# Kernel tuning notes

Measured on AMD Instinct MI355X. Metric: run time of the kernel, lower is better.

## Reference

```python
import jax, jax.numpy as jnp
import numpy as np

B, T, IN, H = 1024, 256, 2, 128
H1, H2, H3 = H // 2, H, 2 * H


def _param(key, shape, fan):
    bound = 1.0 / np.sqrt(fan)
    return jax.random.uniform(key, shape, jnp.float32, -bound, bound)


def setup_inputs() -> dict:
    key = jax.random.key(0)
    ks = jax.random.split(key, 16)
    inp = {
        "input": jax.random.normal(ks[0], (B, T, IN), jnp.float32),
        "future": 16,
        # LSTMCell 1: in=IN, hid=H1 (torch gate order i,f,g,o)
        "W_ih1": _param(ks[1], (4 * H1, IN), H1),
        "W_hh1": _param(ks[2], (4 * H1, H1), H1),
        "b_ih1": _param(ks[3], (4 * H1,), H1),
        "b_hh1": _param(ks[4], (4 * H1,), H1),
        # LSTMCell 2: in=H1, hid=H2
        "W_ih2": _param(ks[5], (4 * H2, H1), H2),
        "W_hh2": _param(ks[6], (4 * H2, H2), H2),
        "b_ih2": _param(ks[7], (4 * H2,), H2),
        "b_hh2": _param(ks[8], (4 * H2,), H2),
        # LSTMCell 3: in=H2, hid=H3
        "W_ih3": _param(ks[9], (4 * H3, H2), H3),
        "W_hh3": _param(ks[10], (4 * H3, H3), H3),
        "b_ih3": _param(ks[11], (4 * H3,), H3),
        "b_hh3": _param(ks[12], (4 * H3,), H3),
        # Linear: (H1+H2+H3) -> IN
        "W_lin": _param(ks[13], (IN, H1 + H2 + H3), H1 + H2 + H3),
        "b_lin": _param(ks[14], (IN,), H1 + H2 + H3),
    }
    return inp


def _lstm_cell(x, h, c, Wih, Whh, bih, bhh):
    g = x @ Wih.T + h @ Whh.T + (bih + bhh)
    i, f, gg, o = jnp.split(g, 4, axis=-1)
    c_new = jax.nn.sigmoid(f) * c + jax.nn.sigmoid(i) * jnp.tanh(gg)
    h_new = jax.nn.sigmoid(o) * jnp.tanh(c_new)
    return h_new, c_new


def reference(input, future, W_ih1, W_hh1, b_ih1, b_hh1,
              W_ih2, W_hh2, b_ih2, b_hh2,
              W_ih3, W_hh3, b_ih3, b_hh3, W_lin, b_lin):
    b = input.shape[0]

    def step(state, x):
        h1, c1, h2, c2, h3, c3 = state
        h1, c1 = _lstm_cell(x, h1, c1, W_ih1, W_hh1, b_ih1, b_hh1)
        h2, c2 = _lstm_cell(h1, h2, c2, W_ih2, W_hh2, b_ih2, b_hh2)
        h3, c3 = _lstm_cell(h2, h3, c3, W_ih3, W_hh3, b_ih3, b_hh3)
        out = jnp.concatenate([h1, h2, h3], axis=-1) @ W_lin.T + b_lin
        return (h1, c1, h2, c2, h3, c3), out

    z = lambda d: jnp.zeros((b, d), input.dtype)
    state0 = (z(H1), z(H1), z(H2), z(H2), z(H3), z(H3))

    # consume the input sequence; only the last output is kept (as in torch code)
    def scan_step(state, x):
        state, out = step(state, x)
        return state, out

    state, outs = jax.lax.scan(scan_step, state0, input.transpose(1, 0, 2))
    out = outs[-1]  # [B, IN]

    def fstep(carry, _):
        state, out = carry
        state, out2 = step(state, out)
        return (state, out2), out2

    (_, _), fouts = jax.lax.scan(fstep, (state, out), None, length=future - 1)
    # stack: first kept output + generated ones -> [B, future, IN]
    return jnp.concatenate([out[:, None, :], fouts.transpose(1, 0, 2)], axis=1)
```

## Files before the change

kernel.cpp:

```cpp
#include <hip/hip_runtime.h>


#define T_SEQ 256
#define NREP 32
#define DEPTH 8
#define DMASK 7

#define NJT1 4
#define NJT2 8
#define NJT3 16
#define NKB1 3
#define NKB2 6
#define NKB3 12

#define WSZ1 (NJT1*4*NKB1*512)
#define WSZ2 (NJT2*8*NKB2*256)
#undef WSZ2
#define WSZ2 (NJT2*4*NKB2*512)
#define WSZ3 (NJT3*4*NKB3*512)
#define WTOT (WSZ1+WSZ2+WSZ3)

#define H2_G    (16*128)
#define H2_SLOT (2*H2_G)
#define H2_REP  (DEPTH*H2_SLOT)
#define H3_G    (16*256)
#define H3_SLOT (2*H3_G)
#define H3_REP  (DEPTH*H3_SLOT)

typedef _Float16 half8 __attribute__((ext_vector_type(8)));
typedef _Float16 half4 __attribute__((ext_vector_type(4)));
typedef float f32x4 __attribute__((ext_vector_type(4)));

union H4u { unsigned long long u; half4 h; };
union H8u { unsigned long long u[2]; half8 h; };

__device__ __forceinline__ float sigm(float x) {
  return __fdividef(1.f, 1.f + __expf(-x));
}
__device__ __forceinline__ float tanh_fast(float x) {
  float t = __expf(-2.f * fabsf(x));
  float r = __fdividef(1.f - t, 1.f + t);
  return copysignf(r, x);
}

__device__ __forceinline__ unsigned long long ld64(const _Float16* p) {
  return __hip_atomic_load((const unsigned long long*)p, __ATOMIC_RELAXED,
                           __HIP_MEMORY_SCOPE_SYSTEM);
}
__device__ __forceinline__ half8 ldh8(const _Float16* p) {
  H8u r; r.u[0] = ld64(p); r.u[1] = ld64(p + 4);
  return r.h;
}
__device__ __forceinline__ void st64(_Float16* p, half4 v) {
  H4u r; r.h = v;
  __hip_atomic_store((unsigned long long*)p, r.u, __ATOMIC_RELAXED,
                     __HIP_MEMORY_SCOPE_SYSTEM);
}
__device__ __forceinline__ void stflag(int* p, int v) {
  __hip_atomic_store(p, v, __ATOMIC_RELAXED, __HIP_MEMORY_SCOPE_SYSTEM);
}
__device__ __forceinline__ void wait_rep(int* fb, int t3, int tf) {
  const int lane = threadIdx.x & 63;
  const bool act = (lane < 4) || ((lane == 4) && (tf != (int)0x80000000));
  int* p = fb + (lane < 5 ? lane : 0) * 64;
  const int tg = (lane < 4) ? t3 : tf;
  while (true) {
    int v = 0x7fffffff;
    if (act) v = __hip_atomic_load(p, __ATOMIC_RELAXED, __HIP_MEMORY_SCOPE_SYSTEM);
    if (__all(v >= tg)) break;
    __builtin_amdgcn_s_sleep(1);
  }
  asm volatile("" ::: "memory");
}

__global__ void prep_weights(const float* __restrict__ Wih1, const float* __restrict__ Whh1,
                             const float* __restrict__ Wih2, const float* __restrict__ Whh2,
                             const float* __restrict__ Wih3, const float* __restrict__ Whh3,
                             _Float16* __restrict__ WT) {
  int idx = blockIdx.x * blockDim.x + threadIdx.x;
  if (idx >= WTOT) return;
  float v = 0.f;
  if (idx < WSZ1) {
    const int e = idx, blk = e >> 9, wb = e & 511;
    const int lane = wb >> 3, j = wb & 7;
    const int tl = blk / NKB1, kk = blk % NKB1;
    const int q = tl / NJT1, jt = tl % NJT1;
    const int r = q * 64 + jt * 16 + (lane & 15);
    const int k = kk * 32 + ((lane >> 4) << 3) + j;
    if (k < 64)       v = Whh1[r * 64 + k];
    else if (k < 66)  v = Wih1[r * 2 + (k - 64)];
  } else if (idx < WSZ1 + WSZ2) {
    const int e = idx - WSZ1, blk = e >> 9, wb = e & 511;
    const int lane = wb >> 3, j = wb & 7;
    const int tl = blk / NKB2, kk = blk % NKB2;
    const int q = tl / NJT2, jt = tl % NJT2;
    const int r = q * 128 + jt * 16 + (lane & 15);
    const int k = kk * 32 + ((lane >> 4) << 3) + j;
    if (k < 64)       v = Wih2[r * 64 + k];
    else              v = Whh2[r * 128 + (k - 64)];
  } else {
    const int e = idx - WSZ1 - WSZ2, blk = e >> 9, wb = e & 511;
    const int lane = wb >> 3, j = wb & 7;
    const int tl = blk / NKB3, kk = blk % NKB3;
    const int q = tl / NJT3, jt = tl % NJT3;
    const int r = q * 256 + jt * 16 + (lane & 15);
    const int k = kk * 32 + ((lane >> 4) << 3) + j;
    if (k < 128)      v = Wih3[r * 128 + k];
    else              v = Whh3[r * 256 + (k - 128)];
  }
  WT[idx] = (_Float16)v;
}

__global__ __launch_bounds__(256, 1) void pipe_main(
    const float* __restrict__ input, const int* __restrict__ future_p,
    const float* __restrict__ bih1, const float* __restrict__ bhh1,
    const float* __restrict__ bih2, const float* __restrict__ bhh2,
    const float* __restrict__ bih3, const float* __restrict__ bhh3,
    const float* __restrict__ Wlin, const float* __restrict__ blin,
    const _Float16* __restrict__ WT,
    _Float16* __restrict__ h2r, _Float16* __restrict__ h3r,
    int* __restrict__ flags,
    float* __restrict__ out) {
  __shared__ __align__(16) _Float16 xh1[2][16][96];
  __shared__ __align__(16) _Float16 xh2[2][16][192];
  __shared__ float wlin[2][448];

  const int fut = *future_p;
  const int nsteps = T_SEQ - 1 + fut;

  const int rep = blockIdx.x % NREP;
  const int role = blockIdx.x / NREP;

  int* fb = flags + rep * 512;
  const int NEG = (int)0x80000000;

  const int tid = threadIdx.x;
  const int w = tid >> 6, lane = tid & 63;
  const int n = lane & 15, l4 = lane >> 4;

  _Float16* h2b = h2r + (size_t)rep * H2_REP;
  _Float16* h3b = h3r + (size_t)rep * H3_REP;

  if (role == 0) {
    for (int i = tid; i < 2*16*96;  i += 256) (&xh1[0][0][0])[i] = (_Float16)0.f;
    for (int i = tid; i < 2*16*192; i += 256) (&xh2[0][0][0])[i] = (_Float16)0.f;
    for (int i = tid; i < 896; i += 256) (&wlin[0][0])[i] = Wlin[i];

    half8 a1[4][3];
#pragma unroll
    for (int q = 0; q < 4; ++q)
#pragma unroll
      for (int kk = 0; kk < 3; ++kk)
        a1[q][kk] = *(const half8*)(WT + ((q*NJT1 + w)*NKB1 + kk)*512 + lane*8);
    half8 a2[2][4][6];
#pragma unroll
    for (int u = 0; u < 2; ++u)
#pragma unroll
      for (int q = 0; q < 4; ++q)
#pragma unroll
        for (int kk = 0; kk < 6; ++kk)
          a2[u][q][kk] = *(const half8*)(WT + WSZ1 + ((q*NJT2 + (u*4+w))*NKB2 + kk)*512 + lane*8);
    float b1[4][4], b2[2][4][4];
#pragma unroll
    for (int q = 0; q < 4; ++q)
#pragma unroll
      for (int e = 0; e < 4; ++e) {
        const int r1 = q*64 + w*16 + l4*4 + e;
        b1[q][e] = bih1[r1] + bhh1[r1];
#pragma unroll
        for (int u = 0; u < 2; ++u) {
          const int r2 = q*128 + (u*4+w)*16 + l4*4 + e;
          b2[u][q][e] = bih2[r2] + bhh2[r2];
        }
      }
    float c1[2][4] = {}, c2[2][2][4] = {};
    __syncthreads();

    for (int it = 0; it <= nsteps; ++it) {
      const int tp = it - 1;
      const int tg3 = (it >= T_SEQ) ? it : it - 6;
      wait_rep(fb, tg3, NEG);

      if (tp >= T_SEQ - 1 && tid < 128) {
        const int kq = tid & 1, ch = (tid >> 1) & 1, nn = (tid >> 2) & 15, gl = (tid >> 6) & 1;
        const _Float16* h3p = h3b + (size_t)(tp & DMASK)*H3_SLOT + gl*H3_G + nn*256;
        float acc = 0.f;
        for (int k = kq*224; k < kq*224 + 224; k += 4) {
          half4 xv;
          if (k < 192) xv = *(const half4*)(&xh2[gl][nn][k]);
          else         { H4u u; u.u = ld64(h3p + (k - 192)); xv = u.h; }
          const float* wl = &wlin[ch][k];
          acc = fmaf(wl[0], (float)xv[0], acc);
          acc = fmaf(wl[1], (float)xv[1], acc);
          acc = fmaf(wl[2], (float)xv[2], acc);
          acc = fmaf(wl[3], (float)xv[3], acc);
        }
        acc += __shfl_xor(acc, 1, 64);
        if (kq == 0) {
          const float o = acc + blin[ch];
          out[((size_t)(rep*32 + gl*16 + nn)*fut + (tp - (T_SEQ - 1)))*2 + ch] = o;
          xh1[gl][nn][64 + ch] = (_Float16)o;
        }
      }
      if (it < T_SEQ && tid < 64) {
        const int gl = tid >> 5, nn = (tid >> 1) & 15, ch = tid & 1;
        xh1[gl][nn][64 + ch] =
            (_Float16)input[((size_t)(rep*32 + gl*16 + nn)*T_SEQ + it)*2 + ch];
      }
      __syncthreads();
      if (it == nsteps) break;

      half8 bf1[2][3];
#pragma unroll
      for (int g = 0; g < 2; ++g)
#pragma unroll
        for (int kk = 0; kk < 3; ++kk)
          bf1[g][kk] = *(const half8*)(&xh1[g][n][kk*32 + l4*8]);
      __syncthreads();
#pragma unroll
      for (int g = 0; g < 2; ++g) {
        f32x4 acc[4];
#pragma unroll
        for (int q = 0; q < 4; ++q)
#pragma unroll
          for (int e = 0; e < 4; ++e) acc[q][e] = b1[q][e];
#pragma unroll
        for (int q = 0; q < 4; ++q)
#pragma unroll
          for (int kk = 0; kk < 3; ++kk)
            acc[q] = __builtin_amdgcn_mfma_f32_16x16x32_f16(a1[q][kk], bf1[g][kk], acc[q], 0, 0, 0);
        half4 hv;
#pragma unroll
        for (int e = 0; e < 4; ++e) {
          const float cn = sigm(acc[1][e]) * c1[g][e] + sigm(acc[0][e]) * tanh_fast(acc[2][e]);
          const float h = sigm(acc[3][e]) * tanh_fast(cn);
          c1[g][e] = cn;
          hv[e] = (_Float16)h;
        }
        *(half4*)(&xh1[g][n][w*16 + l4*4]) = hv;
        *(half4*)(&xh2[g][n][w*16 + l4*4]) = hv;
      }
      __syncthreads();

      half8 bf2[2][6];
#pragma unroll
      for (int g = 0; g < 2; ++g)
#pragma unroll
        for (int kk = 0; kk < 6; ++kk)
          bf2[g][kk] = *(const half8*)(&xh2[g][n][kk*32 + l4*8]);
      __syncthreads();
      const int slot = it & DMASK;
#pragma unroll
      for (int u = 0; u < 2; ++u)
#pragma unroll
        for (int g = 0; g < 2; ++g) {
          f32x4 acc[4];
#pragma unroll
          for (int q = 0; q < 4; ++q)
#pragma unroll
            for (int e = 0; e < 4; ++e) acc[q][e] = b2[u][q][e];
#pragma unroll
          for (int q = 0; q < 4; ++q)
#pragma unroll
            for (int kk = 0; kk < 6; ++kk)
              acc[q] = __builtin_amdgcn_mfma_f32_16x16x32_f16(a2[u][q][kk], bf2[g][kk], acc[q], 0, 0, 0);
          half4 hv;
#pragma unroll
          for (int e = 0; e < 4; ++e) {
            const float cn = sigm(acc[1][e]) * c2[u][g][e] + sigm(acc[0][e]) * tanh_fast(acc[2][e]);
            const float h = sigm(acc[3][e]) * tanh_fast(cn);
            c2[u][g][e] = cn;
            hv[e] = (_Float16)h;
          }
          const int row = (u*4 + w)*16 + l4*4;
          *(half4*)(&xh2[g][n][64 + row]) = hv;
          st64(h2b + (size_t)slot*H2_SLOT + g*H2_G + n*128 + row, hv);
        }
      asm volatile("s_waitcnt vmcnt(0)" ::: "memory");
      __syncthreads();
      if (tid == 0) stflag(fb + 4*64, it + 1);
    }
  } else {
    const int slice = role - 1;
    const int tl = slice*4 + w;
    half8 a3[4][12];
#pragma unroll
    for (int q = 0; q < 4; ++q)
#pragma unroll
      for (int kk = 0; kk < 12; ++kk)
        a3[q][kk] = *(const half8*)(WT + WSZ1 + WSZ2 + ((q*NJT3 + tl)*NKB3 + kk)*512 + lane*8);
    float b3[4][4];
#pragma unroll
    for (int q = 0; q < 4; ++q)
#pragma unroll
      for (int e = 0; e < 4; ++e) {
        const int r = q*256 + tl*16 + l4*4 + e;
        b3[q][e] = bih3[r] + bhh3[r];
      }
    float c3[2][4] = {};

    for (int t = 0; t < nsteps; ++t) {
      wait_rep(fb, t, t + 1);
      const int slot = t & DMASK, slot1 = (t - 1) & DMASK;
      half8 bf[2][12];
#pragma unroll
      for (int g = 0; g < 2; ++g) {
        const _Float16* h2p = h2b + (size_t)slot*H2_SLOT + g*H2_G + n*128;
#pragma unroll
        for (int kk = 0; kk < 4; ++kk) bf[g][kk] = ldh8(h2p + kk*32 + l4*8);
        if (t > 0) {
          const _Float16* h3p = h3b + (size_t)slot1*H3_SLOT + g*H3_G + n*256;
#pragma unroll
          for (int kk = 4; kk < 12; ++kk) bf[g][kk] = ldh8(h3p + (kk-4)*32 + l4*8);
        } else {
#pragma unroll
          for (int kk = 4; kk < 12; ++kk) bf[g][kk] = half8{};
        }
      }
#pragma unroll
      for (int g = 0; g < 2; ++g) {
        f32x4 acc[4];
#pragma unroll
        for (int q = 0; q < 4; ++q)
#pragma unroll
          for (int e = 0; e < 4; ++e) acc[q][e] = b3[q][e];
#pragma unroll
        for (int q = 0; q < 4; ++q)
#pragma unroll
          for (int kk = 0; kk < 12; ++kk)
            acc[q] = __builtin_amdgcn_mfma_f32_16x16x32_f16(a3[q][kk], bf[g][kk], acc[q], 0, 0, 0);
        half4 hv;
#pragma unroll
        for (int e = 0; e < 4; ++e) {
          const float cn = sigm(acc[1][e]) * c3[g][e] + sigm(acc[0][e]) * tanh_fast(acc[2][e]);
          const float h = sigm(acc[3][e]) * tanh_fast(cn);
          c3[g][e] = cn;
          hv[e] = (_Float16)h;
        }
        st64(h3b + (size_t)slot*H3_SLOT + g*H3_G + n*256 + tl*16 + l4*4, hv);
      }
      asm volatile("s_waitcnt vmcnt(0)" ::: "memory");
      __syncthreads();
      if (tid == 0) stflag(fb + slice*64, t + 1);
    }
  }
}

extern "C" void kernel_launch(void* const* d_in, const int* in_sizes, int n_in,
                              void* d_out, int out_size, void* d_ws, size_t ws_size,
                              hipStream_t stream) {
  const float* input = (const float*)d_in[0];
  const int*   fut   = (const int*)d_in[1];
  const float* Wih1  = (const float*)d_in[2];
  const float* Whh1  = (const float*)d_in[3];
  const float* bih1  = (const float*)d_in[4];
  const float* bhh1  = (const float*)d_in[5];
  const float* Wih2  = (const float*)d_in[6];
  const float* Whh2  = (const float*)d_in[7];
  const float* bih2  = (const float*)d_in[8];
  const float* bhh2  = (const float*)d_in[9];
  const float* Wih3  = (const float*)d_in[10];
  const float* Whh3  = (const float*)d_in[11];
  const float* bih3  = (const float*)d_in[12];
  const float* bhh3  = (const float*)d_in[13];
  const float* Wlin  = (const float*)d_in[14];
  const float* blin  = (const float*)d_in[15];
  float* out = (float*)d_out;

  _Float16* WT  = (_Float16*)d_ws;
  _Float16* h2r = WT + WTOT;
  _Float16* h3r = h2r + (size_t)NREP * H2_REP;
  int* flags    = (int*)(h3r + (size_t)NREP * H3_REP);
  const size_t flag_bytes = (size_t)NREP * 512 * sizeof(int);

  prep_weights<<<(WTOT + 255) / 256, 256, 0, stream>>>(Wih1, Whh1, Wih2, Whh2, Wih3, Whh3, WT);
  hipMemsetAsync(flags, 0, flag_bytes, stream);
  pipe_main<<<5 * NREP, 256, 0, stream>>>(input, fut,
                                          bih1, bhh1, bih2, bhh2, bih3, bhh3,
                                          Wlin, blin, WT, h2r, h3r, flags, out);
}
```

Before: 2.267 ms.

## Split layer-3 across two sibling blocks per team with LDS staging and partial linear

Reorganizes the pipelined LSTM from five blocks per replica (one layer-1/2 block plus four layer-3 slices) to three blocks per team, where two blocks each own half of layer 3 with doubled MFMA tiles per wave. The h3 state each block produced is kept in LDS, and the sibling half is staged through shared memory. Each layer-3 block computes its part of the output linear and publishes it for the layer-1/2 block to combine. Flag waits for layer 1/2 are batched every 4 steps, and a spin cap with a dead flag is added. This lowers inter-block flag traffic and the number of global h3 loads, at the cost of heavier per-block work and extra __syncthreads.

```diff
diff --git a/kernel.cpp b/kernel.cpp
--- a/kernel.cpp
+++ b/kernel.cpp
@@ -2,9 +2,8 @@
 
 
 #define T_SEQ 256
-#define NREP 32
-#define DEPTH 8
-#define DMASK 7
+#define NTEAM 32
+#define G2 2
 
 #define NJT1 4
 #define NJT2 8
@@ -14,25 +13,22 @@
 #define NKB3 12
 
 #define WSZ1 (NJT1*4*NKB1*512)
-#define WSZ2 (NJT2*8*NKB2*256)
-#undef WSZ2
 #define WSZ2 (NJT2*4*NKB2*512)
 #define WSZ3 (NJT3*4*NKB3*512)
 #define WTOT (WSZ1+WSZ2+WSZ3)
 
-#define H2_G    (16*128)
-#define H2_SLOT (2*H2_G)
-#define H2_REP  (DEPTH*H2_SLOT)
-#define H3_G    (16*256)
-#define H3_SLOT (2*H3_G)
-#define H3_REP  (DEPTH*H3_SLOT)
+#define H2SLOT 4096
+#define H2TEAM (8*H2SLOT)
+#define H3SLOT 8192
+#define H3TEAM (4*H3SLOT)
+#define PRTEAM 512
+#define CAP_WAIT (1<<22)
 
 typedef _Float16 half8 __attribute__((ext_vector_type(8)));
 typedef _Float16 half4 __attribute__((ext_vector_type(4)));
 typedef float f32x4 __attribute__((ext_vector_type(4)));
 
 union H4u { unsigned long long u; half4 h; };
-union H8u { unsigned long long u[2]; half8 h; };
 
 __device__ __forceinline__ float sigm(float x) {
   return __fdividef(1.f, 1.f + __expf(-x));
@@ -43,34 +39,43 @@
   return copysignf(r, x);
 }
 
-__device__ __forceinline__ unsigned long long ld64(const _Float16* p) {
+__device__ __forceinline__ unsigned long long ld64p(const _Float16* p) {
   return __hip_atomic_load((const unsigned long long*)p, __ATOMIC_RELAXED,
                            __HIP_MEMORY_SCOPE_SYSTEM);
 }
-__device__ __forceinline__ half8 ldh8(const _Float16* p) {
-  H8u r; r.u[0] = ld64(p); r.u[1] = ld64(p + 4);
-  return r.h;
-}
-__device__ __forceinline__ void st64(_Float16* p, half4 v) {
+__device__ __forceinline__ void st64p(_Float16* p, half4 v) {
   H4u r; r.h = v;
   __hip_atomic_store((unsigned long long*)p, r.u, __ATOMIC_RELAXED,
                      __HIP_MEMORY_SCOPE_SYSTEM);
 }
+__device__ __forceinline__ float ldfp(const float* p) {
+  return __hip_atomic_load(p, __ATOMIC_RELAXED, __HIP_MEMORY_SCOPE_SYSTEM);
+}
+__device__ __forceinline__ void stfp(float* p, float v) {
+  __hip_atomic_store(p, v, __ATOMIC_RELAXED, __HIP_MEMORY_SCOPE_SYSTEM);
+}
 __device__ __forceinline__ void stflag(int* p, int v) {
-  __hip_atomic_store(p, v, __ATOMIC_RELAXED, __HIP_MEMORY_SCOPE_SYSTEM);
-}
-__device__ __forceinline__ void wait_rep(int* fb, int t3, int tf) {
+  __hip_atomic_store(p, v, __ATOMIC_RELEASE, __HIP_MEMORY_SCOPE_SYSTEM);
+}
+__device__ __forceinline__ void wait2(const int* pA, int tA, const int* pB, int tB,
+                                      volatile int* dead) {
+  if (*dead) return;
   const int lane = threadIdx.x & 63;
-  const bool act = (lane < 4) || ((lane == 4) && (tf != (int)0x80000000));
-  int* p = fb + (lane < 5 ? lane : 0) * 64;
-  const int tg = (lane < 4) ? t3 : tf;
+  const int* p = (lane == 1) ? pB : pA;
+  const int tg = (lane == 0) ? tA : (lane == 1 ? tB : (int)0x80000000);
+  int iter = 0;
   while (true) {
-    int v = 0x7fffffff;
-    if (act) v = __hip_atomic_load(p, __ATOMIC_RELAXED, __HIP_MEMORY_SCOPE_SYSTEM);
+    const int v = (lane < 2)
+        ? __hip_atomic_load(p, __ATOMIC_RELAXED, __HIP_MEMORY_SCOPE_SYSTEM)
+        : 0x7fffffff;
     if (__all(v >= tg)) break;
+    if (++iter > CAP_WAIT) { if (lane == 0) *dead = 1; break; }
     __builtin_amdgcn_s_sleep(1);
   }
   asm volatile("" ::: "memory");
+}
+__device__ __forceinline__ void vm0() {
+  asm volatile("s_waitcnt vmcnt(0)" ::: "memory");
 }
 
 __global__ void prep_weights(const float* __restrict__ Wih1, const float* __restrict__ Whh1,
@@ -119,32 +124,42 @@
     const float* __restrict__ Wlin, const float* __restrict__ blin,
     const _Float16* __restrict__ WT,
     _Float16* __restrict__ h2r, _Float16* __restrict__ h3r,
-    int* __restrict__ flags,
+    float* __restrict__ pr, int* __restrict__ flags,
     float* __restrict__ out) {
-  __shared__ __align__(16) _Float16 xh1[2][16][96];
-  __shared__ __align__(16) _Float16 xh2[2][16][192];
-  __shared__ float wlin[2][448];
-
-  const int fut = *future_p;
-  const int nsteps = T_SEQ - 1 + fut;
-
-  const int rep = blockIdx.x % NREP;
-  const int role = blockIdx.x / NREP;
-
-  int* fb = flags + rep * 512;
-  const int NEG = (int)0x80000000;
-
   const int tid = threadIdx.x;
   const int w = tid >> 6, lane = tid & 63;
   const int n = lane & 15, l4 = lane >> 4;
 
-  _Float16* h2b = h2r + (size_t)rep * H2_REP;
-  _Float16* h3b = h3r + (size_t)rep * H3_REP;
+  const int team = blockIdx.x & 31;
+  const int role = blockIdx.x >> 5;
+  const int b0 = team * 32;
+
+  const int fut = *future_p;
+  const int nsteps = T_SEQ - 1 + fut;
+
+  int* fbase = flags + team * 192;
+  int* fA = fbase;
+  int* fB = fbase + 64;
+  int* fF = fbase + 128;
+  _Float16* h2b = h2r + (size_t)team * H2TEAM;
+  _Float16* h3b = h3r + (size_t)team * H3TEAM;
+  float* prb = pr + (size_t)team * PRTEAM;
+
+  __shared__ volatile int sh_dead;
+  if (tid == 0) sh_dead = 0;
 
   if (role == 0) {
-    for (int i = tid; i < 2*16*96;  i += 256) (&xh1[0][0][0])[i] = (_Float16)0.f;
-    for (int i = tid; i < 2*16*192; i += 256) (&xh2[0][0][0])[i] = (_Float16)0.f;
-    for (int i = tid; i < 896; i += 256) (&wlin[0][0])[i] = Wlin[i];
+    __shared__ __align__(16) _Float16 xh1s[G2][16][104];
+    __shared__ __align__(16) _Float16 xh2s[G2][16][200];
+    __shared__ float bs1[256], bs2[512], wlinF[2][192], blin_s[2];
+
+    for (int i = tid; i < G2*16*104; i += 256) (&xh1s[0][0][0])[i] = (_Float16)0.f;
+    for (int i = tid; i < G2*16*200; i += 256) (&xh2s[0][0][0])[i] = (_Float16)0.f;
+    if (tid < 256) bs1[tid] = bih1[tid] + bhh1[tid];
+    bs2[tid] = bih2[tid] + bhh2[tid];
+    bs2[tid + 256] = bih2[tid + 256] + bhh2[tid + 256];
+    if (tid < 192) { wlinF[0][tid] = Wlin[tid]; wlinF[1][tid] = Wlin[448 + tid]; }
+    if (tid < 2) blin_s[tid] = blin[tid];
 
     half8 a1[4][3];
 #pragma unroll
@@ -160,70 +175,57 @@
 #pragma unroll
         for (int kk = 0; kk < 6; ++kk)
           a2[u][q][kk] = *(const half8*)(WT + WSZ1 + ((q*NJT2 + (u*4+w))*NKB2 + kk)*512 + lane*8);
-    float b1[4][4], b2[2][4][4];
-#pragma unroll
-    for (int q = 0; q < 4; ++q)
-#pragma unroll
-      for (int e = 0; e < 4; ++e) {
-        const int r1 = q*64 + w*16 + l4*4 + e;
-        b1[q][e] = bih1[r1] + bhh1[r1];
-#pragma unroll
-        for (int u = 0; u < 2; ++u) {
-          const int r2 = q*128 + (u*4+w)*16 + l4*4 + e;
-          b2[u][q][e] = bih2[r2] + bhh2[r2];
-        }
-      }
-    float c1[2][4] = {}, c2[2][2][4] = {};
+    float c1[G2][4] = {}, c2[2][G2][4] = {};
     __syncthreads();
 
     for (int it = 0; it <= nsteps; ++it) {
       const int tp = it - 1;
-      const int tg3 = (it >= T_SEQ) ? it : it - 6;
-      wait_rep(fb, tg3, NEG);
-
-      if (tp >= T_SEQ - 1 && tid < 128) {
-        const int kq = tid & 1, ch = (tid >> 1) & 1, nn = (tid >> 2) & 15, gl = (tid >> 6) & 1;
-        const _Float16* h3p = h3b + (size_t)(tp & DMASK)*H3_SLOT + gl*H3_G + nn*256;
+      if (it >= T_SEQ)        wait2(fA, it, fB, it, &sh_dead);
+      else if ((it & 3) == 0) wait2(fA, it - 4, fB, it - 4, &sh_dead);
+
+      if (tp >= T_SEQ - 1) {
+        const int g = w >> 1, ch = w & 1;
+        const int kq = l4;
         float acc = 0.f;
-        for (int k = kq*224; k < kq*224 + 224; k += 4) {
-          half4 xv;
-          if (k < 192) xv = *(const half4*)(&xh2[gl][nn][k]);
-          else         { H4u u; u.u = ld64(h3p + (k - 192)); xv = u.h; }
-          const float* wl = &wlin[ch][k];
+#pragma unroll
+        for (int i = 0; i < 12; ++i) {
+          const int k = kq*48 + i*4;
+          const half4 xv = *(const half4*)(&xh2s[g][n][k]);
+          const float* wl = &wlinF[ch][k];
           acc = fmaf(wl[0], (float)xv[0], acc);
           acc = fmaf(wl[1], (float)xv[1], acc);
           acc = fmaf(wl[2], (float)xv[2], acc);
           acc = fmaf(wl[3], (float)xv[3], acc);
         }
-        acc += __shfl_xor(acc, 1, 64);
-        if (kq == 0) {
-          const float o = acc + blin[ch];
-          out[((size_t)(rep*32 + gl*16 + nn)*fut + (tp - (T_SEQ - 1)))*2 + ch] = o;
-          xh1[gl][nn][64 + ch] = (_Float16)o;
+        acc += __shfl_xor(acc, 16, 64);
+        acc += __shfl_xor(acc, 32, 64);
+        if (l4 == 0) {
+          const float* pp = prb + (tp & 3)*128 + g*32 + n*2 + ch;
+          const float o = acc + blin_s[ch] + ldfp(pp) + ldfp(pp + 64);
+          out[((size_t)(b0 + g*16 + n)*fut + (tp - (T_SEQ - 1)))*2 + ch] = o;
+          xh1s[g][n][64 + ch] = (_Float16)o;
         }
       }
       if (it < T_SEQ && tid < 64) {
-        const int gl = tid >> 5, nn = (tid >> 1) & 15, ch = tid & 1;
-        xh1[gl][nn][64 + ch] =
-            (_Float16)input[((size_t)(rep*32 + gl*16 + nn)*T_SEQ + it)*2 + ch];
+        const int g = tid >> 5, nn = (tid >> 1) & 15, ch = tid & 1;
+        xh1s[g][nn][64 + ch] =
+            (_Float16)input[((size_t)(b0 + g*16 + nn)*T_SEQ + it)*2 + ch];
       }
       __syncthreads();
       if (it == nsteps) break;
 
-      half8 bf1[2][3];
-#pragma unroll
-      for (int g = 0; g < 2; ++g)
+      half8 bf1[G2][3];
+#pragma unroll
+      for (int g = 0; g < G2; ++g)
 #pragma unroll
         for (int kk = 0; kk < 3; ++kk)
-          bf1[g][kk] = *(const half8*)(&xh1[g][n][kk*32 + l4*8]);
-      __syncthreads();
-#pragma unroll
-      for (int g = 0; g < 2; ++g) {
+          bf1[g][kk] = *(const half8*)(&xh1s[g][n][kk*32 + l4*8]);
+      __syncthreads();
+#pragma unroll
+      for (int g = 0; g < G2; ++g) {
         f32x4 acc[4];
 #pragma unroll
-        for (int q = 0; q < 4; ++q)
-#pragma unroll
-          for (int e = 0; e < 4; ++e) acc[q][e] = b1[q][e];
+        for (int q = 0; q < 4; ++q) acc[q] = *(const f32x4*)(&bs1[q*64 + w*16 + l4*4]);
 #pragma unroll
         for (int q = 0; q < 4; ++q)
 #pragma unroll
@@ -237,28 +239,27 @@
           c1[g][e] = cn;
           hv[e] = (_Float16)h;
         }
-        *(half4*)(&xh1[g][n][w*16 + l4*4]) = hv;
-        *(half4*)(&xh2[g][n][w*16 + l4*4]) = hv;
-      }
-      __syncthreads();
-
-      half8 bf2[2][6];
-#pragma unroll
-      for (int g = 0; g < 2; ++g)
+        *(half4*)(&xh1s[g][n][w*16 + l4*4]) = hv;
+        *(half4*)(&xh2s[g][n][w*16 + l4*4]) = hv;
+      }
+      __syncthreads();
+
+      half8 bf2[G2][6];
+#pragma unroll
+      for (int g = 0; g < G2; ++g)
 #pragma unroll
         for (int kk = 0; kk < 6; ++kk)
-          bf2[g][kk] = *(const half8*)(&xh2[g][n][kk*32 + l4*8]);
-      __syncthreads();
-      const int slot = it & DMASK;
+          bf2[g][kk] = *(const half8*)(&xh2s[g][n][kk*32 + l4*8]);
+      __syncthreads();
+      const int slot = it & 7;
 #pragma unroll
       for (int u = 0; u < 2; ++u)
 #pragma unroll
-        for (int g = 0; g < 2; ++g) {
+        for (int g = 0; g < G2; ++g) {
           f32x4 acc[4];
 #pragma unroll
           for (int q = 0; q < 4; ++q)
-#pragma unroll
-            for (int e = 0; e < 4; ++e) acc[q][e] = b2[u][q][e];
+            acc[q] = *(const f32x4*)(&bs2[q*128 + (u*4+w)*16 + l4*4]);
 #pragma unroll
           for (int q = 0; q < 4; ++q)
 #pragma unroll
@@ -273,75 +274,134 @@
             hv[e] = (_Float16)h;
           }
           const int row = (u*4 + w)*16 + l4*4;
-          *(half4*)(&xh2[g][n][64 + row]) = hv;
-          st64(h2b + (size_t)slot*H2_SLOT + g*H2_G + n*128 + row, hv);
-        }
-      asm volatile("s_waitcnt vmcnt(0)" ::: "memory");
-      __syncthreads();
-      if (tid == 0) stflag(fb + 4*64, it + 1);
+          *(half4*)(&xh2s[g][n][64 + row]) = hv;
+          st64p(h2b + (size_t)slot*H2SLOT + g*2048 + n*128 + row, hv);
+        }
+      vm0();
+      __syncthreads();
+      if (tid == 0) stflag(fF, it + 1);
     }
   } else {
-    const int slice = role - 1;
-    const int tl = slice*4 + w;
-    half8 a3[4][12];
-#pragma unroll
-    for (int q = 0; q < 4; ++q)
-#pragma unroll
-      for (int kk = 0; kk < 12; ++kk)
-        a3[q][kk] = *(const half8*)(WT + WSZ1 + WSZ2 + ((q*NJT3 + tl)*NKB3 + kk)*512 + lane*8);
-    float b3[4][4];
-#pragma unroll
-    for (int q = 0; q < 4; ++q)
-#pragma unroll
-      for (int e = 0; e < 4; ++e) {
-        const int r = q*256 + tl*16 + l4*4 + e;
-        b3[q][e] = bih3[r] + bhh3[r];
-      }
-    float c3[2][4] = {};
+    const int h = role - 1, hs = 1 - h;
+    __shared__ __align__(16) _Float16 stage[G2][16][264];
+    __shared__ __align__(16) _Float16 xh3own[G2][16][132];
+    __shared__ float bs3s[4][2][4][16];
+    __shared__ float wlp[2][128];
+
+    for (int i = tid; i < G2*16*264; i += 256) (&stage[0][0][0])[i] = (_Float16)0.f;
+    for (int i = tid; i < G2*16*132; i += 256) (&xh3own[0][0][0])[i] = (_Float16)0.f;
+    {
+      int i = tid;
+#pragma unroll
+      for (int rnd = 0; rnd < 2; ++rnd, i += 256) {
+        const int w2 = i >> 7, u = (i >> 6) & 1, q = (i >> 4) & 3, col = i & 15;
+        const int r = q*256 + (h*8 + w2*2 + u)*16 + col;
+        bs3s[w2][u][q][col] = bih3[r] + bhh3[r];
+      }
+    }
+    if (tid < 256) {
+      const int ch = tid >> 7, k = tid & 127;
+      wlp[ch][k] = Wlin[ch*448 + 192 + h*128 + k];
+    }
+    half8 a3[2][4][12];
+#pragma unroll
+    for (int u = 0; u < 2; ++u)
+#pragma unroll
+      for (int q = 0; q < 4; ++q)
+#pragma unroll
+        for (int kk = 0; kk < 12; ++kk)
+          a3[u][q][kk] = *(const half8*)(WT + WSZ1 + WSZ2 +
+              ((q*NJT3 + (h*8 + w*2 + u))*NKB3 + kk)*512 + lane*8);
+    float c3[G2][2][4] = {};
+    int* fme  = h ? fB : fA;
+    int* fsib = h ? fA : fB;
+    __syncthreads();
 
     for (int t = 0; t < nsteps; ++t) {
-      wait_rep(fb, t, t + 1);
-      const int slot = t & DMASK, slot1 = (t - 1) & DMASK;
-      half8 bf[2][12];
-#pragma unroll
-      for (int g = 0; g < 2; ++g) {
-        const _Float16* h2p = h2b + (size_t)slot*H2_SLOT + g*H2_G + n*128;
-#pragma unroll
-        for (int kk = 0; kk < 4; ++kk) bf[g][kk] = ldh8(h2p + kk*32 + l4*8);
-        if (t > 0) {
-          const _Float16* h3p = h3b + (size_t)slot1*H3_SLOT + g*H3_G + n*256;
-#pragma unroll
-          for (int kk = 4; kk < 12; ++kk) bf[g][kk] = ldh8(h3p + (kk-4)*32 + l4*8);
-        } else {
-#pragma unroll
-          for (int kk = 4; kk < 12; ++kk) bf[g][kk] = half8{};
-        }
-      }
-#pragma unroll
-      for (int g = 0; g < 2; ++g) {
-        f32x4 acc[4];
-#pragma unroll
-        for (int q = 0; q < 4; ++q)
-#pragma unroll
-          for (int e = 0; e < 4; ++e) acc[q][e] = b3[q][e];
-#pragma unroll
-        for (int q = 0; q < 4; ++q)
-#pragma unroll
-          for (int kk = 0; kk < 12; ++kk)
-            acc[q] = __builtin_amdgcn_mfma_f32_16x16x32_f16(a3[q][kk], bf[g][kk], acc[q], 0, 0, 0);
-        half4 hv;
-#pragma unroll
-        for (int e = 0; e < 4; ++e) {
-          const float cn = sigm(acc[1][e]) * c3[g][e] + sigm(acc[0][e]) * tanh_fast(acc[2][e]);
-          const float h = sigm(acc[3][e]) * tanh_fast(cn);
-          c3[g][e] = cn;
-          hv[e] = (_Float16)h;
-        }
-        st64(h3b + (size_t)slot*H3_SLOT + g*H3_G + n*256 + tl*16 + l4*4, hv);
-      }
-      asm volatile("s_waitcnt vmcnt(0)" ::: "memory");
-      __syncthreads();
-      if (tid == 0) stflag(fb + slice*64, t + 1);
+      wait2(fsib, t, fF, t + 1, &sh_dead);
+      const int s2 = t & 7, s3 = (t - 1) & 3;
+#pragma unroll
+      for (int g = 0; g < G2; ++g) {
+        half8 bfo[4];
+#pragma unroll
+        for (int s = 0; s < 4; ++s)
+          bfo[s] = *(const half8*)(&xh3own[g][n][s*32 + l4*8]);
+#pragma unroll
+        for (int j = 0; j < 2; ++j) {
+          const int kst = 2*w + j;
+          H4u v0, v1;
+          if (kst < 4) {
+            const _Float16* p = h2b + (size_t)s2*H2SLOT + g*2048 + n*128 + kst*32 + l4*8;
+            v0.u = ld64p(p); v1.u = ld64p(p + 4);
+          } else if (t > 0) {
+            const _Float16* p = h3b + (size_t)s3*H3SLOT + hs*4096 + g*2048 + n*128
+                              + (kst - 4)*32 + l4*8;
+            v0.u = ld64p(p); v1.u = ld64p(p + 4);
+          } else { v0.u = 0; v1.u = 0; }
+          *(half4*)(&stage[g][n][kst*32 + l4*8]) = v0.h;
+          *(half4*)(&stage[g][n][kst*32 + l4*8 + 4]) = v1.h;
+        }
+        __syncthreads();
+        half8 bf[12];
+#pragma unroll
+        for (int s = 0; s < 4; ++s) {
+          bf[s] = *(const half8*)(&stage[g][n][s*32 + l4*8]);
+          bf[4 + 4*h + s] = bfo[s];
+          bf[4 + 4*hs + s] = *(const half8*)(&stage[g][n][128 + s*32 + l4*8]);
+        }
+        f32x4 acc[2][4];
+#pragma unroll
+        for (int u = 0; u < 2; ++u)
+#pragma unroll
+          for (int q = 0; q < 4; ++q)
+            acc[u][q] = *(const f32x4*)(&bs3s[w][u][q][l4*4]);
+#pragma unroll
+        for (int u = 0; u < 2; ++u)
+#pragma unroll
+          for (int q = 0; q < 4; ++q)
+#pragma unroll
+            for (int kk = 0; kk < 12; ++kk)
+              acc[u][q] = __builtin_amdgcn_mfma_f32_16x16x32_f16(a3[u][q][kk], bf[kk], acc[u][q], 0, 0, 0);
+#pragma unroll
+        for (int u = 0; u < 2; ++u) {
+          half4 hv;
+#pragma unroll
+          for (int e = 0; e < 4; ++e) {
+            const float cn = sigm(acc[u][1][e]) * c3[g][u][e]
+                           + sigm(acc[u][0][e]) * tanh_fast(acc[u][2][e]);
+            const float hh = sigm(acc[u][3][e]) * tanh_fast(cn);
+            c3[g][u][e] = cn;
+            hv[e] = (_Float16)hh;
+          }
+          const int c = (w*2 + u)*16 + l4*4;
+          *(half4*)(&xh3own[g][n][c]) = hv;
+          st64p(h3b + (size_t)(t & 3)*H3SLOT + h*4096 + g*2048 + n*128 + c, hv);
+        }
+        __syncthreads();
+      }
+      vm0();
+      __syncthreads();
+      if (t >= T_SEQ - 1) {
+        const int g = w >> 1, ch = w & 1;
+        float pa = 0.f;
+#pragma unroll
+        for (int i = 0; i < 8; ++i) {
+          const int k = l4*32 + i*4;
+          const half4 xv = *(const half4*)(&xh3own[g][n][k]);
+          const float* wl = &wlp[ch][k];
+          pa = fmaf(wl[0], (float)xv[0], pa);
+          pa = fmaf(wl[1], (float)xv[1], pa);
+          pa = fmaf(wl[2], (float)xv[2], pa);
+          pa = fmaf(wl[3], (float)xv[3], pa);
+        }
+        pa += __shfl_xor(pa, 16, 64);
+        pa += __shfl_xor(pa, 32, 64);
+        if (l4 == 0)
+          stfp(prb + (t & 3)*128 + h*64 + g*32 + n*2 + ch, pa);
+        vm0();
+        __syncthreads();
+      }
+      if (tid == 0) stflag(fme, t + 1);
     }
   }
 }
@@ -369,13 +429,14 @@
 
   _Float16* WT  = (_Float16*)d_ws;
   _Float16* h2r = WT + WTOT;
-  _Float16* h3r = h2r + (size_t)NREP * H2_REP;
-  int* flags    = (int*)(h3r + (size_t)NREP * H3_REP);
-  const size_t flag_bytes = (size_t)NREP * 512 * sizeof(int);
+  _Float16* h3r = h2r + (size_t)NTEAM * H2TEAM;
+  float*    pr  = (float*)(h3r + (size_t)NTEAM * H3TEAM);
+  int*    flags = (int*)(pr + (size_t)NTEAM * PRTEAM);
+  const size_t flag_bytes = (size_t)NTEAM * 192 * sizeof(int);
 
   prep_weights<<<(WTOT + 255) / 256, 256, 0, stream>>>(Wih1, Whh1, Wih2, Whh2, Wih3, Whh3, WT);
   hipMemsetAsync(flags, 0, flag_bytes, stream);
-  pipe_main<<<5 * NREP, 256, 0, stream>>>(input, fut,
-                                          bih1, bhh1, bih2, bhh2, bih3, bhh3,
-                                          Wlin, blin, WT, h2r, h3r, flags, out);
-}
+  pipe_main<<<96, 256, 0, stream>>>(input, fut,
+                                    bih1, bhh1, bih2, bhh2, bih3, bhh3,
+                                    Wlin, blin, WT, h2r, h3r, pr, flags, out);
+}
```

Result: slower. 3.656 ms (+61.3%).

## Regroup pipeline into 16 teams of 64 rows with per-wave flags and layer-3 partial projections

Applied to the files above, without the earlier changes.

Replaces 32 replicas of 32 batch rows with 16 teams of 64 rows, so each block handles four 16-row groups. The grid shrinks from 160 to 80 blocks and per-team weight-load overhead is amortized over more rows. Layer-3 blocks now double-buffer their global h2/h3 loads across groups and compute the output-projection partials for their own h3 slice. This removes the serial 448-wide dot product from the layer-1/2 block. Synchronization moves to per-wave flags with a bounded wait cap, and the ring depth and lookahead drop from 8/6 to 4/3. The trade-off is more serial work per block on fewer CUs, and a wait cap that can silently give up on a stalled producer.

```diff
diff --git a/kernel.cpp b/kernel.cpp
--- a/kernel.cpp
+++ b/kernel.cpp
@@ -2,9 +2,9 @@
 
 
 #define T_SEQ 256
-#define NREP 32
-#define DEPTH 8
-#define DMASK 7
+#define NTEAM 16
+#define G4 4
+#define DEPTH 4
 
 #define NJT1 4
 #define NJT2 8
@@ -12,20 +12,16 @@
 #define NKB1 3
 #define NKB2 6
 #define NKB3 12
-
 #define WSZ1 (NJT1*4*NKB1*512)
-#define WSZ2 (NJT2*8*NKB2*256)
-#undef WSZ2
 #define WSZ2 (NJT2*4*NKB2*512)
 #define WSZ3 (NJT3*4*NKB3*512)
 #define WTOT (WSZ1+WSZ2+WSZ3)
 
-#define H2_G    (16*128)
-#define H2_SLOT (2*H2_G)
-#define H2_REP  (DEPTH*H2_SLOT)
-#define H3_G    (16*256)
-#define H3_SLOT (2*H3_G)
-#define H3_REP  (DEPTH*H3_SLOT)
+#define H2_TEAM (G4*DEPTH*2048)
+#define H3_TEAM (G4*DEPTH*4096)
+#define PR_TEAM (G4*DEPTH*4*32)
+#define FL_TEAM 1088
+#define CAP_WAIT (1<<22)
 
 typedef _Float16 half8 __attribute__((ext_vector_type(8)));
 typedef _Float16 half4 __attribute__((ext_vector_type(4)));
@@ -43,31 +39,37 @@
   return copysignf(r, x);
 }
 
-__device__ __forceinline__ unsigned long long ld64(const _Float16* p) {
+__device__ __forceinline__ unsigned long long ld64p(const _Float16* p) {
   return __hip_atomic_load((const unsigned long long*)p, __ATOMIC_RELAXED,
                            __HIP_MEMORY_SCOPE_SYSTEM);
 }
-__device__ __forceinline__ half8 ldh8(const _Float16* p) {
-  H8u r; r.u[0] = ld64(p); r.u[1] = ld64(p + 4);
-  return r.h;
-}
-__device__ __forceinline__ void st64(_Float16* p, half4 v) {
+__device__ __forceinline__ void st64p(_Float16* p, half4 v) {
   H4u r; r.h = v;
   __hip_atomic_store((unsigned long long*)p, r.u, __ATOMIC_RELAXED,
                      __HIP_MEMORY_SCOPE_SYSTEM);
 }
+__device__ __forceinline__ float ldfp(const float* p) {
+  return __hip_atomic_load(p, __ATOMIC_RELAXED, __HIP_MEMORY_SCOPE_SYSTEM);
+}
+__device__ __forceinline__ void stfp(float* p, float v) {
+  __hip_atomic_store(p, v, __ATOMIC_RELAXED, __HIP_MEMORY_SCOPE_SYSTEM);
+}
 __device__ __forceinline__ void stflag(int* p, int v) {
   __hip_atomic_store(p, v, __ATOMIC_RELAXED, __HIP_MEMORY_SCOPE_SYSTEM);
 }
-__device__ __forceinline__ void wait_rep(int* fb, int t3, int tf) {
+__device__ __forceinline__ void vm0() {
+  asm volatile("s_waitcnt vmcnt(0)" ::: "memory");
+}
+__device__ __forceinline__ void waitq(const int* ft, int tg3, int tgF, int* dead) {
+  if (*dead) return;
   const int lane = threadIdx.x & 63;
-  const bool act = (lane < 4) || ((lane == 4) && (tf != (int)0x80000000));
-  int* p = fb + (lane < 5 ? lane : 0) * 64;
-  const int tg = (lane < 4) ? t3 : tf;
+  const int* p = ft + ((lane < 17) ? lane : 0) * 64;
+  const int tg = (lane < 16) ? tg3 : (lane == 16 ? tgF : (int)0x80000000);
+  int it = 0;
   while (true) {
-    int v = 0x7fffffff;
-    if (act) v = __hip_atomic_load(p, __ATOMIC_RELAXED, __HIP_MEMORY_SCOPE_SYSTEM);
+    const int v = __hip_atomic_load(p, __ATOMIC_RELAXED, __HIP_MEMORY_SCOPE_SYSTEM);
     if (__all(v >= tg)) break;
+    if (++it > CAP_WAIT) { *dead = 1; break; }
     __builtin_amdgcn_s_sleep(1);
   }
   asm volatile("" ::: "memory");
@@ -111,6 +113,63 @@
   WT[idx] = (_Float16)v;
 }
 
+#define LOADQ(bf, g, t)                                                        \
+  {                                                                            \
+    const _Float16* p2_ = h2b + (((g)*DEPTH + ((t)&3)) << 11) + n*128 + l4*8;  \
+    _Pragma("unroll")                                                          \
+    for (int kk_ = 0; kk_ < 4; ++kk_) {                                        \
+      H8u u_; u_.u[0] = ld64p(p2_ + kk_*32); u_.u[1] = ld64p(p2_ + kk_*32 + 4);\
+      bf[kk_] = u_.h;                                                          \
+    }                                                                          \
+    if ((t) > 0) {                                                             \
+      const _Float16* p3_ = h3b + (((g)*DEPTH + (((t)-1)&3)) << 12)            \
+                          + n*256 + l4*8;                                      \
+      _Pragma("unroll")                                                        \
+      for (int s_ = 0; s_ < 8; ++s_) {                                         \
+        H8u u_; u_.u[0] = ld64p(p3_ + s_*32); u_.u[1] = ld64p(p3_ + s_*32 + 4);\
+        bf[4 + s_] = u_.h;                                                     \
+      }                                                                        \
+    } else {                                                                   \
+      _Pragma("unroll")                                                        \
+      for (int s_ = 0; s_ < 8; ++s_) bf[4 + s_] = half8{};                     \
+    }                                                                          \
+  }
+
+#define COMPUTEQ(bf, g, t, futp)                                               \
+  {                                                                            \
+    f32x4 acc_[4];                                                             \
+    _Pragma("unroll")                                                          \
+    for (int q_ = 0; q_ < 4; ++q_)                                             \
+      _Pragma("unroll")                                                        \
+      for (int e_ = 0; e_ < 4; ++e_) acc_[q_][e_] = b3r[q_][e_];               \
+    _Pragma("unroll")                                                          \
+    for (int q_ = 0; q_ < 4; ++q_)                                             \
+      _Pragma("unroll")                                                        \
+      for (int kk_ = 0; kk_ < 12; ++kk_)                                       \
+        acc_[q_] = __builtin_amdgcn_mfma_f32_16x16x32_f16(a3[q_][kk_], bf[kk_],\
+                                                          acc_[q_], 0, 0, 0); \
+    half4 hv_; float hf_[4];                                                   \
+    _Pragma("unroll")                                                          \
+    for (int e_ = 0; e_ < 4; ++e_) {                                           \
+      const float cn_ = sigm(acc_[1][e_]) * c3[g][e_]                          \
+                      + sigm(acc_[0][e_]) * tanh_fast(acc_[2][e_]);            \
+      hf_[e_] = sigm(acc_[3][e_]) * tanh_fast(cn_);                            \
+      c3[g][e_] = cn_;                                                         \
+      hv_[e_] = (_Float16)hf_[e_];                                             \
+    }                                                                          \
+    st64p(h3b + (((g)*DEPTH + ((t)&3)) << 12) + n*256 + tl*16 + l4*4, hv_);    \
+    if (futp) {                                                                \
+      float p0_ = 0.f, p1_ = 0.f;                                              \
+      _Pragma("unroll")                                                        \
+      for (int e_ = 0; e_ < 4; ++e_) {                                         \
+        p0_ = fmaf(wle[0][e_], hf_[e_], p0_);                                  \
+        p1_ = fmaf(wle[1][e_], hf_[e_], p1_);                                  \
+      }                                                                        \
+      part[g][n][0][(w << 2) | l4] = p0_;                                      \
+      part[g][n][1][(w << 2) | l4] = p1_;                                      \
+    }                                                                          \
+  }
+
 __global__ __launch_bounds__(256, 1) void pipe_main(
     const float* __restrict__ input, const int* __restrict__ future_p,
     const float* __restrict__ bih1, const float* __restrict__ bhh1,
@@ -119,32 +178,34 @@
     const float* __restrict__ Wlin, const float* __restrict__ blin,
     const _Float16* __restrict__ WT,
     _Float16* __restrict__ h2r, _Float16* __restrict__ h3r,
-    int* __restrict__ flags,
+    float* __restrict__ pr, int* __restrict__ flags,
     float* __restrict__ out) {
-  __shared__ __align__(16) _Float16 xh1[2][16][96];
-  __shared__ __align__(16) _Float16 xh2[2][16][192];
-  __shared__ float wlin[2][448];
-
-  const int fut = *future_p;
-  const int nsteps = T_SEQ - 1 + fut;
-
-  const int rep = blockIdx.x % NREP;
-  const int role = blockIdx.x / NREP;
-
-  int* fb = flags + rep * 512;
-  const int NEG = (int)0x80000000;
+  __shared__ __align__(16) _Float16 xh1s[G4][16][104];
+  __shared__ __align__(16) _Float16 xh2s[G4][16][200];
+  __shared__ float wlinF[2][192];
+  __shared__ float part[G4][16][2][16];
 
   const int tid = threadIdx.x;
   const int w = tid >> 6, lane = tid & 63;
   const int n = lane & 15, l4 = lane >> 4;
-
-  _Float16* h2b = h2r + (size_t)rep * H2_REP;
-  _Float16* h3b = h3r + (size_t)rep * H3_REP;
+  const int team = blockIdx.x % NTEAM;
+  const int role = blockIdx.x / NTEAM;
+  const int b0 = team * 64;
+  const int fut = *future_p;
+  const int nsteps = T_SEQ - 1 + fut;
+  int* ft = flags + team * FL_TEAM;
+  int* flf = ft + 16 * 64;
+  _Float16* h2b = h2r + (size_t)team * H2_TEAM;
+  _Float16* h3b = h3r + (size_t)team * H3_TEAM;
+  float* prb = pr + (size_t)team * PR_TEAM;
+  int dead = 0;
+  const int NEG = (int)0x80000000;
 
   if (role == 0) {
-    for (int i = tid; i < 2*16*96;  i += 256) (&xh1[0][0][0])[i] = (_Float16)0.f;
-    for (int i = tid; i < 2*16*192; i += 256) (&xh2[0][0][0])[i] = (_Float16)0.f;
-    for (int i = tid; i < 896; i += 256) (&wlin[0][0])[i] = Wlin[i];
+    for (int i = tid; i < G4*16*104; i += 256) (&xh1s[0][0][0])[i] = (_Float16)0.f;
+    for (int i = tid; i < G4*16*200; i += 256) (&xh2s[0][0][0])[i] = (_Float16)0.f;
+    for (int i = tid; i < 384; i += 256)
+      wlinF[i / 192][i % 192] = Wlin[(i / 192) * 448 + (i % 192)];
 
     half8 a1[4][3];
 #pragma unroll
@@ -160,70 +221,69 @@
 #pragma unroll
         for (int kk = 0; kk < 6; ++kk)
           a2[u][q][kk] = *(const half8*)(WT + WSZ1 + ((q*NJT2 + (u*4+w))*NKB2 + kk)*512 + lane*8);
-    float b1[4][4], b2[2][4][4];
+    float b1r[4][4], b2r[2][4][4];
 #pragma unroll
     for (int q = 0; q < 4; ++q)
 #pragma unroll
       for (int e = 0; e < 4; ++e) {
         const int r1 = q*64 + w*16 + l4*4 + e;
-        b1[q][e] = bih1[r1] + bhh1[r1];
+        b1r[q][e] = bih1[r1] + bhh1[r1];
 #pragma unroll
         for (int u = 0; u < 2; ++u) {
           const int r2 = q*128 + (u*4+w)*16 + l4*4 + e;
-          b2[u][q][e] = bih2[r2] + bhh2[r2];
+          b2r[u][q][e] = bih2[r2] + bhh2[r2];
         }
       }
-    float c1[2][4] = {}, c2[2][2][4] = {};
+    float c1[G4][4] = {}, c2[2][G4][4] = {};
     __syncthreads();
 
     for (int it = 0; it <= nsteps; ++it) {
       const int tp = it - 1;
-      const int tg3 = (it >= T_SEQ) ? it : it - 6;
-      wait_rep(fb, tg3, NEG);
+      waitq(ft, (it >= T_SEQ) ? it : it - 3, NEG, &dead);
 
       if (tp >= T_SEQ - 1 && tid < 128) {
-        const int kq = tid & 1, ch = (tid >> 1) & 1, nn = (tid >> 2) & 15, gl = (tid >> 6) & 1;
-        const _Float16* h3p = h3b + (size_t)(tp & DMASK)*H3_SLOT + gl*H3_G + nn*256;
+        const int g = tid >> 5, nn = (tid >> 1) & 15, ch = tid & 1;
         float acc = 0.f;
-        for (int k = kq*224; k < kq*224 + 224; k += 4) {
-          half4 xv;
-          if (k < 192) xv = *(const half4*)(&xh2[gl][nn][k]);
-          else         { H4u u; u.u = ld64(h3p + (k - 192)); xv = u.h; }
-          const float* wl = &wlin[ch][k];
+#pragma unroll
+        for (int i = 0; i < 48; ++i) {
+          const int k = i * 4;
+          const half4 xv = *(const half4*)(&xh2s[g][nn][k]);
+          const float* wl = &wlinF[ch][k];
           acc = fmaf(wl[0], (float)xv[0], acc);
           acc = fmaf(wl[1], (float)xv[1], acc);
           acc = fmaf(wl[2], (float)xv[2], acc);
           acc = fmaf(wl[3], (float)xv[3], acc);
         }
-        acc += __shfl_xor(acc, 1, 64);
-        if (kq == 0) {
-          const float o = acc + blin[ch];
-          out[((size_t)(rep*32 + gl*16 + nn)*fut + (tp - (T_SEQ - 1)))*2 + ch] = o;
-          xh1[gl][nn][64 + ch] = (_Float16)o;
-        }
-      }
-      if (it < T_SEQ && tid < 64) {
-        const int gl = tid >> 5, nn = (tid >> 1) & 15, ch = tid & 1;
-        xh1[gl][nn][64 + ch] =
-            (_Float16)input[((size_t)(rep*32 + gl*16 + nn)*T_SEQ + it)*2 + ch];
-      }
+        const int sl = tp & 3;
+#pragma unroll
+        for (int q = 0; q < 4; ++q)
+          acc += ldfp(prb + ((g*DEPTH + sl)*4 + q)*32 + nn*2 + ch);
+        const float o = acc + blin[ch];
+        out[((size_t)(b0 + g*16 + nn)*fut + (tp - (T_SEQ - 1)))*2 + ch] = o;
+        xh1s[g][nn][64 + ch] = (_Float16)o;
+      }
+      if (it < T_SEQ && tid < 128) {
+        const int g = tid >> 5, nn = (tid >> 1) & 15, ch = tid & 1;
+        xh1s[g][nn][64 + ch] =
+            (_Float16)input[((size_t)(b0 + g*16 + nn)*T_SEQ + it)*2 + ch];
+      }
+      if (it == nsteps) break;
       __syncthreads();
-      if (it == nsteps) break;
-
-      half8 bf1[2][3];
-#pragma unroll
-      for (int g = 0; g < 2; ++g)
+
+      half8 bf1[G4][3];
+#pragma unroll
+      for (int g = 0; g < G4; ++g)
 #pragma unroll
         for (int kk = 0; kk < 3; ++kk)
-          bf1[g][kk] = *(const half8*)(&xh1[g][n][kk*32 + l4*8]);
+          bf1[g][kk] = *(const half8*)(&xh1s[g][n][kk*32 + l4*8]);
       __syncthreads();
 #pragma unroll
-      for (int g = 0; g < 2; ++g) {
+      for (int g = 0; g < G4; ++g) {
         f32x4 acc[4];
 #pragma unroll
         for (int q = 0; q < 4; ++q)
 #pragma unroll
-          for (int e = 0; e < 4; ++e) acc[q][e] = b1[q][e];
+          for (int e = 0; e < 4; ++e) acc[q][e] = b1r[q][e];
 #pragma unroll
         for (int q = 0; q < 4; ++q)
 #pragma unroll
@@ -237,28 +297,28 @@
           c1[g][e] = cn;
           hv[e] = (_Float16)h;
         }
-        *(half4*)(&xh1[g][n][w*16 + l4*4]) = hv;
-        *(half4*)(&xh2[g][n][w*16 + l4*4]) = hv;
+        *(half4*)(&xh1s[g][n][w*16 + l4*4]) = hv;
+        *(half4*)(&xh2s[g][n][w*16 + l4*4]) = hv;
       }
       __syncthreads();
 
-      half8 bf2[2][6];
-#pragma unroll
-      for (int g = 0; g < 2; ++g)
+      half8 bf2[G4][6];
+#pragma unroll
+      for (int g = 0; g < G4; ++g)
 #pragma unroll
         for (int kk = 0; kk < 6; ++kk)
-          bf2[g][kk] = *(const half8*)(&xh2[g][n][kk*32 + l4*8]);
+          bf2[g][kk] = *(const half8*)(&xh2s[g][n][kk*32 + l4*8]);
       __syncthreads();
-      const int slot = it & DMASK;
+      const int slot = it & 3;
 #pragma unroll
       for (int u = 0; u < 2; ++u)
 #pragma unroll
-        for (int g = 0; g < 2; ++g) {
+        for (int g = 0; g < G4; ++g) {
           f32x4 acc[4];
 #pragma unroll
           for (int q = 0; q < 4; ++q)
 #pragma unroll
-            for (int e = 0; e < 4; ++e) acc[q][e] = b2[u][q][e];
+            for (int e = 0; e < 4; ++e) acc[q][e] = b2r[u][q][e];
 #pragma unroll
           for (int q = 0; q < 4; ++q)
 #pragma unroll
@@ -273,75 +333,66 @@
             hv[e] = (_Float16)h;
           }
           const int row = (u*4 + w)*16 + l4*4;
-          *(half4*)(&xh2[g][n][64 + row]) = hv;
-          st64(h2b + (size_t)slot*H2_SLOT + g*H2_G + n*128 + row, hv);
+          *(half4*)(&xh2s[g][n][64 + row]) = hv;
+          st64p(h2b + ((g*DEPTH + slot) << 11) + n*128 + row, hv);
         }
-      asm volatile("s_waitcnt vmcnt(0)" ::: "memory");
+      vm0();
       __syncthreads();
-      if (tid == 0) stflag(fb + 4*64, it + 1);
+      if (tid == 0) stflag(flf, it + 1);
     }
   } else {
-    const int slice = role - 1;
-    const int tl = slice*4 + w;
+    const int qh = role - 1;
+    const int tl = qh*4 + w;
     half8 a3[4][12];
 #pragma unroll
     for (int q = 0; q < 4; ++q)
 #pragma unroll
       for (int kk = 0; kk < 12; ++kk)
         a3[q][kk] = *(const half8*)(WT + WSZ1 + WSZ2 + ((q*NJT3 + tl)*NKB3 + kk)*512 + lane*8);
-    float b3[4][4];
+    float b3r[4][4], wle[2][4];
 #pragma unroll
     for (int q = 0; q < 4; ++q)
 #pragma unroll
       for (int e = 0; e < 4; ++e) {
         const int r = q*256 + tl*16 + l4*4 + e;
-        b3[q][e] = bih3[r] + bhh3[r];
-      }
-    float c3[2][4] = {};
+        b3r[q][e] = bih3[r] + bhh3[r];
+      }
+#pragma unroll
+    for (int ch = 0; ch < 2; ++ch)
+#pragma unroll
+      for (int e = 0; e < 4; ++e)
+        wle[ch][e] = Wlin[ch*448 + 192 + tl*16 + l4*4 + e];
+    float c3[G4][4] = {};
+    half8 bfA[12], bfB[12];
 
     for (int t = 0; t < nsteps; ++t) {
-      wait_rep(fb, t, t + 1);
-      const int slot = t & DMASK, slot1 = (t - 1) & DMASK;
-      half8 bf[2][12];
-#pragma unroll
-      for (int g = 0; g < 2; ++g) {
-        const _Float16* h2p = h2b + (size_t)slot*H2_SLOT + g*H2_G + n*128;
-#pragma unroll
-        for (int kk = 0; kk < 4; ++kk) bf[g][kk] = ldh8(h2p + kk*32 + l4*8);
-        if (t > 0) {
-          const _Float16* h3p = h3b + (size_t)slot1*H3_SLOT + g*H3_G + n*256;
-#pragma unroll
-          for (int kk = 4; kk < 12; ++kk) bf[g][kk] = ldh8(h3p + (kk-4)*32 + l4*8);
-        } else {
-#pragma unroll
-          for (int kk = 4; kk < 12; ++kk) bf[g][kk] = half8{};
+      waitq(ft, t, t + 1, &dead);
+      const bool futp = (t >= T_SEQ - 1);
+
+      LOADQ(bfA, 0, t);
+      LOADQ(bfB, 1, t);
+      __builtin_amdgcn_sched_barrier(0);
+      COMPUTEQ(bfA, 0, t, futp);
+      LOADQ(bfA, 2, t);
+      __builtin_amdgcn_sched_barrier(0);
+      COMPUTEQ(bfB, 1, t, futp);
+      LOADQ(bfB, 3, t);
+      __builtin_amdgcn_sched_barrier(0);
+      COMPUTEQ(bfA, 2, t, futp);
+      COMPUTEQ(bfB, 3, t, futp);
+
+      if (futp) {
+        __syncthreads();
+        if (tid < 128) {
+          const int g = tid >> 5, nn = (tid >> 1) & 15, ch = tid & 1;
+          float s = 0.f;
+#pragma unroll
+          for (int j = 0; j < 16; ++j) s += part[g][nn][ch][j];
+          stfp(prb + ((g*DEPTH + (t & 3))*4 + qh)*32 + nn*2 + ch, s);
         }
       }
-#pragma unroll
-      for (int g = 0; g < 2; ++g) {
-        f32x4 acc[4];
-#pragma unroll
-        for (int q = 0; q < 4; ++q)
-#pragma unroll
-          for (int e = 0; e < 4; ++e) acc[q][e] = b3[q][e];
-#pragma unroll
-        for (int q = 0; q < 4; ++q)
-#pragma unroll
-          for (int kk = 0; kk < 12; ++kk)
-            acc[q] = __builtin_amdgcn_mfma_f32_16x16x32_f16(a3[q][kk], bf[g][kk], acc[q], 0, 0, 0);
-        half4 hv;
-#pragma unroll
-        for (int e = 0; e < 4; ++e) {
-          const float cn = sigm(acc[1][e]) * c3[g][e] + sigm(acc[0][e]) * tanh_fast(acc[2][e]);
-          const float h = sigm(acc[3][e]) * tanh_fast(cn);
-          c3[g][e] = cn;
-          hv[e] = (_Float16)h;
-        }
-        st64(h3b + (size_t)slot*H3_SLOT + g*H3_G + n*256 + tl*16 + l4*4, hv);
-      }
-      asm volatile("s_waitcnt vmcnt(0)" ::: "memory");
-      __syncthreads();
-      if (tid == 0) stflag(fb + slice*64, t + 1);
+      vm0();
+      if (lane == 0) stflag(ft + tl*64, t + 1);
     }
   }
 }
@@ -369,13 +420,14 @@
 
   _Float16* WT  = (_Float16*)d_ws;
   _Float16* h2r = WT + WTOT;
-  _Float16* h3r = h2r + (size_t)NREP * H2_REP;
-  int* flags    = (int*)(h3r + (size_t)NREP * H3_REP);
-  const size_t flag_bytes = (size_t)NREP * 512 * sizeof(int);
+  _Float16* h3r = h2r + (size_t)NTEAM * H2_TEAM;
+  float*    pr  = (float*)(h3r + (size_t)NTEAM * H3_TEAM);
+  int*    flags = (int*)(pr + (size_t)NTEAM * PR_TEAM);
+  const size_t flag_bytes = (size_t)NTEAM * FL_TEAM * sizeof(int);
 
   prep_weights<<<(WTOT + 255) / 256, 256, 0, stream>>>(Wih1, Whh1, Wih2, Whh2, Wih3, Whh3, WT);
   hipMemsetAsync(flags, 0, flag_bytes, stream);
-  pipe_main<<<5 * NREP, 256, 0, stream>>>(input, fut,
-                                          bih1, bhh1, bih2, bhh2, bih3, bhh3,
-                                          Wlin, blin, WT, h2r, h3r, flags, out);
-}
+  pipe_main<<<5 * NTEAM, 256, 0, stream>>>(input, fut,
+                                           bih1, bhh1, bih2, bhh2, bih3, bhh3,
+                                           Wlin, blin, WT, h2r, h3r, pr, flags, out);
+}
```

Result: slower. 3.940 ms (+73.8%).
